# Kernel optimization log

Hardware: AMD Instinct MI355X
Metric: run time of the kernel (lower is better)

The kernel has to match this reference:

```python
import jax, jax.numpy as jnp
import numpy as np

B, T, DIM, H = 4, 2048, 1024, 16
NOPE, ROPE, VDIM, KVR = 128, 64, 128, 512
QKD = NOPE + ROPE  # 192
SCALE = QKD ** -0.5
THETA = 10000.0


def apply_rope(x, cos, sin):
    # x: (B, T, H, D) with interleaved (real, imag) pairs; cos/sin: (T, D//2)
    xr, xi = x[..., 0::2], x[..., 1::2]
    c = cos[None, :, None, :]
    s = sin[None, :, None, :]
    yr = xr * c - xi * s
    yi = xr * s + xi * c
    return jnp.stack([yr, yi], axis=-1).reshape(x.shape)


def rms_norm(x, eps=1e-6):
    return x * jax.lax.rsqrt(jnp.mean(x * x, axis=-1, keepdims=True) + eps)


def setup_inputs() -> dict:
    key = jax.random.key(0)
    ks = jax.random.split(key, 10)
    def lin(k, fan_in, fan_out):
        bound = 1.0 / np.sqrt(fan_in)
        kw, kb = jax.random.split(k)
        w = jax.random.uniform(kw, (fan_out, fan_in), jnp.float32, -bound, bound)
        b = jax.random.uniform(kb, (fan_out,), jnp.float32, -bound, bound)
        return w, b
    wq_w, wq_b = lin(ks[0], DIM, H * QKD)
    wkv_a_w, wkv_a_b = lin(ks[1], DIM, KVR + ROPE)
    wkv_b_w, wkv_b_b = lin(ks[2], KVR, H * (NOPE + VDIM))
    wo_w, wo_b = lin(ks[3], H * VDIM, DIM)
    x = jax.random.normal(ks[4], (B, T, DIM), jnp.float32)
    inv_freq = THETA ** (-jnp.arange(0, ROPE, 2, dtype=jnp.float32) / ROPE)  # (32,)
    ang = jnp.arange(T, dtype=jnp.float32)[:, None] * inv_freq[None, :]  # (T, 32)
    return {
        "x": x,
        "wq_w": wq_w, "wq_b": wq_b,
        "wkv_a_w": wkv_a_w, "wkv_a_b": wkv_a_b,
        "wkv_b_w": wkv_b_w, "wkv_b_b": wkv_b_b,
        "wo_w": wo_w, "wo_b": wo_b,
        "freqs_cos": jnp.cos(ang), "freqs_sin": jnp.sin(ang),
        "start_pos": 0,
    }


def reference(x, wq_w, wq_b, wkv_a_w, wkv_a_b, wkv_b_w, wkv_b_b, wo_w, wo_b,
              freqs_cos, freqs_sin, start_pos):
    b, t, _ = x.shape
    # Q projection, split into nope + rope parts
    q = (x @ wq_w.T + wq_b).reshape(b, t, H, QKD)
    q_nope, q_rope = q[..., :NOPE], q[..., NOPE:]
    q_rope = apply_rope(q_rope, freqs_cos, freqs_sin)
    q = jnp.concatenate([q_nope, q_rope], axis=-1)  # (B,T,H,192)
    # low-rank KV latent + shared rope key
    kv_a = x @ wkv_a_w.T + wkv_a_b  # (B,T,576)
    kv_lat, k_rope = kv_a[..., :KVR], kv_a[..., KVR:]
    k_rope = apply_rope(k_rope[:, :, None, :], freqs_cos, freqs_sin)  # (B,T,1,64)
    # decompress latent -> k_nope, v
    kv = (rms_norm(kv_lat) @ wkv_b_w.T + wkv_b_b).reshape(b, t, H, NOPE + VDIM)
    k_nope, v = kv[..., :NOPE], kv[..., NOPE:]
    k = jnp.concatenate([k_nope, jnp.broadcast_to(k_rope, (b, t, H, ROPE))], axis=-1)
    # causal SDPA (start_pos=0 prefill: cache[:end_pos] == current k/v)
    scores = jnp.einsum("bthd,bshd->bhts", q, k) * SCALE
    causal = jnp.tril(jnp.ones((t, t), dtype=bool))
    scores = jnp.where(causal[None, None], scores, jnp.finfo(scores.dtype).min)
    probs = jax.nn.softmax(scores, axis=-1)
    out = jnp.einsum("bhts,bshd->bthd", probs, v).reshape(b, t, H * VDIM)
    return out @ wo_w.T + wo_b
```

## Files before the change

### kernel.cpp

```cpp
#include <hip/hip_runtime.h>
#include <hip/hip_bf16.h>
#include <cmath>

#define B_    4
#define T_    2048
#define DIM_  1024
#define H_    16
#define NOPE_ 128
#define ROPE_ 64
#define VDIM_ 128
#define KVR_  512
#define QKD_  192
#define NTOK  (B_ * T_)

static constexpr float SCALE2_ = 0.07216878364870322f * 1.4426950408889634f;

typedef __attribute__((ext_vector_type(8))) unsigned short ushort8_t;
typedef __bf16 v8bf __attribute__((ext_vector_type(8)));
typedef float  v4f  __attribute__((ext_vector_type(4)));
typedef unsigned int v4u __attribute__((ext_vector_type(4)));

__device__ __forceinline__ float bf2f(unsigned short u) {
    return __uint_as_float(((unsigned int)u) << 16);
}
__device__ __forceinline__ unsigned short f2bf(float f) {
    unsigned int u = __float_as_uint(f);
    u += 0x7FFFu + ((u >> 16) & 1u);
    return (unsigned short)(u >> 16);
}
__device__ __forceinline__ unsigned short f2bf_hw(float f) {
    return __builtin_bit_cast(unsigned short, (__bf16)f);
}
__device__ __forceinline__ unsigned int cvt_pk_bf16(float lo, float hi) {
    unsigned int r;
    asm("v_cvt_pk_bf16_f32 %0, %1, %2" : "=v"(r) : "v"(lo), "v"(hi));
    return r;
}
__device__ __forceinline__ void store1(float* p, float v)          { *p = v; }
__device__ __forceinline__ void store1(__hip_bfloat16* p, float v) { *p = __float2bfloat16(v); }

__device__ __forceinline__ float exp2_hw(float x) {
    return __builtin_amdgcn_exp2f(x);
}

__device__ __forceinline__ void load_lds16(const void* g, void* l) {
    __builtin_amdgcn_global_load_lds(
        (const __attribute__((address_space(1))) void*)g,
        (__attribute__((address_space(3))) void*)l, 16, 0, 0);
}

__device__ __forceinline__ void cvt4(const float* s, __hip_bfloat16* d, int q4) {
    const int i = q4 * 4;
    const float4 v = *(const float4*)(s + i);
    ushort4 o;
    o.x = f2bf(v.x); o.y = f2bf(v.y); o.z = f2bf(v.z); o.w = f2bf(v.w);
    *(ushort4*)((unsigned short*)d + i) = o;
}

#define X4_   (NTOK*1024/4)
#define Q4_   (3072*1024/4)
#define KB4_  (4096*512/4)
#define O4_   (1024*2048/4)
#define A4_   (640*1024/4)
#define CVT_TOTAL (X4_ + Q4_ + KB4_ + O4_ + A4_)

__global__ __launch_bounds__(256) void cvt_all(
    const float* __restrict__ x,    const float* __restrict__ wq,
    const float* __restrict__ wkvb, const float* __restrict__ wo,
    const float* __restrict__ wkva, const float* __restrict__ wkva_bias,
    __hip_bfloat16* __restrict__ xb,    __hip_bfloat16* __restrict__ wqb,
    __hip_bfloat16* __restrict__ wkvbb, __hip_bfloat16* __restrict__ wob,
    __hip_bfloat16* __restrict__ wkvab, float* __restrict__ bias_pad)
{
    int idx = blockIdx.x * 256 + threadIdx.x;
    if (idx < X4_) { cvt4(x, xb, idx); return; }
    idx -= X4_;
    if (idx < Q4_) { cvt4(wq, wqb, idx); return; }
    idx -= Q4_;
    if (idx < KB4_) { cvt4(wkvb, wkvbb, idx); return; }
    idx -= KB4_;
    if (idx < O4_) { cvt4(wo, wob, idx); return; }
    idx -= O4_;
    if (idx < A4_) {
        const int i = idx * 4;
        ushort4 o;
        if (i < 576 * 1024) {
            const float4 v = *(const float4*)(wkva + i);
            o.x = f2bf(v.x); o.y = f2bf(v.y); o.z = f2bf(v.z); o.w = f2bf(v.w);
        } else {
            o.x = o.y = o.z = o.w = 0;
        }
        *(ushort4*)((unsigned short*)wkvab + i) = o;
        if (idx < 640) bias_pad[idx] = (idx < 576) ? wkva_bias[idx] : 0.0f;
    }
}

template <typename CT, int EPI>
__global__ __launch_bounds__(256) void gemm_mfma(
    const __hip_bfloat16* __restrict__ A, int lda,
    const __hip_bfloat16* __restrict__ W, int ldw,
    const float* __restrict__ bias,
    CT* __restrict__ C, int ldc, int K,
    unsigned short* __restrict__ kvf)
{
    __shared__ unsigned short smem[2 * 128 * 32];
    unsigned short* A_s = smem;
    unsigned short* B_s = smem + 128 * 32;

    const int tid  = threadIdx.x;
    const int ln   = tid & 63;
    const int wv   = tid >> 6;
    const int l15  = ln & 15;
    const int quad = ln >> 4;
    const int wm   = wv & 1, wn = wv >> 1;
    const int n0 = blockIdx.x * 128, m0 = blockIdx.y * 128;

    v4f acc[4][4] = {};

    for (int k0 = 0; k0 < K; k0 += 32) {
        __syncthreads();
        #pragma unroll
        for (int it = 0; it < 2; ++it) {
            const int idx = it * 256 + wv * 64;
            const int li  = idx + ln;
            const int row = li >> 2, ch = li & 3;
            load_lds16(A + (size_t)(m0 + row) * lda + k0 + ch * 8, &A_s[idx * 8]);
            load_lds16(W + (size_t)(n0 + row) * ldw + k0 + ch * 8, &B_s[idx * 8]);
        }
        __syncthreads();

        v8bf af[4], bf_[4];
        #pragma unroll
        for (int i = 0; i < 4; ++i) {
            af[i]  = *(const v8bf*)&A_s[(wm * 64 + i * 16 + l15) * 32 + quad * 8];
            bf_[i] = *(const v8bf*)&B_s[(wn * 64 + i * 16 + l15) * 32 + quad * 8];
        }
        #pragma unroll
        for (int i = 0; i < 4; ++i)
            #pragma unroll
            for (int j = 0; j < 4; ++j)
                acc[i][j] = __builtin_amdgcn_mfma_f32_16x16x32_bf16(
                                af[i], bf_[j], acc[i][j], 0, 0, 0);
    }

    if (EPI == 0) {
        #pragma unroll
        for (int i = 0; i < 4; ++i) {
            const int mrow = m0 + wm * 64 + i * 16 + quad * 4;
            #pragma unroll
            for (int j = 0; j < 4; ++j) {
                const int ncol = n0 + wn * 64 + j * 16 + l15;
                const float bb = bias[ncol];
                #pragma unroll
                for (int r = 0; r < 4; ++r)
                    store1(C + (size_t)(mrow + r) * ldc + ncol, acc[i][j][r] + bb);
            }
        }
    } else {
        const int head = n0 >> 8;
        const bool is_v = (n0 & 128) != 0;
        __syncthreads();
        #pragma unroll
        for (int p = 0; p < 2; ++p) {
            if (p) __syncthreads();
            if (wm == p) {
                #pragma unroll
                for (int i = 0; i < 4; ++i) {
                    #pragma unroll
                    for (int j = 0; j < 4; ++j) {
                        const int ncl = wn * 64 + j * 16 + l15;
                        const float bb = bias[n0 + ncl];
                        #pragma unroll
                        for (int r = 0; r < 4; ++r) {
                            const unsigned short v = f2bf(acc[i][j][r] + bb);
                            const int lnf = quad * 4 + r;
                            int off;
                            if (!is_v) {
                                const int s = ncl >> 5, qf = (ncl >> 3) & 3, e = ncl & 7;
                                off = (s * 4 + i) * 512 + (qf * 16 + lnf) * 8 + e;
                            } else {
                                const int nt = ncl >> 4, lnv = ncl & 15;
                                const int jj = i * 16 + lnf;
                                const int s2 = jj >> 5, qv = (jj >> 3) & 3, ev = jj & 7;
                                off = (nt * 2 + s2) * 512 + (qv * 16 + lnv) * 8 + ev;
                            }
                            smem[off] = v;
                        }
                    }
                }
            }
            __syncthreads();
            const size_t GT = (size_t)(m0 >> 6) + p;
            unsigned short* dst = kvf + ((GT * 16 + head) << 14) + (is_v ? 16 * 512 : 0);
            #pragma unroll
            for (int it = 0; it < 4; ++it) {
                const int u = (tid + it * 256) * 8;
                *(ushort8_t*)(dst + u) = *(const ushort8_t*)&smem[u];
            }
        }
    }
}

__global__ __launch_bounds__(256) void gemm_qkva(
    const __hip_bfloat16* __restrict__ A,
    const __hip_bfloat16* __restrict__ Wq, const float* __restrict__ biasq,
    __hip_bfloat16* __restrict__ Cq,
    const __hip_bfloat16* __restrict__ Wa, const float* __restrict__ biasa,
    __hip_bfloat16* __restrict__ Ca)
{
    __shared__ unsigned short smem[2 * 128 * 32];
    unsigned short* A_s = smem;
    unsigned short* B_s = smem + 128 * 32;

    const bool is_q = blockIdx.x < 24;
    const __hip_bfloat16* W = is_q ? Wq : Wa;
    const float* bias       = is_q ? biasq : biasa;
    __hip_bfloat16* C       = is_q ? Cq : Ca;
    const int ldc = is_q ? 3072 : 640;
    const int n0  = (is_q ? blockIdx.x : (blockIdx.x - 24)) * 128;
    const int m0  = blockIdx.y * 128;

    const int tid  = threadIdx.x;
    const int ln   = tid & 63;
    const int wv   = tid >> 6;
    const int l15  = ln & 15;
    const int quad = ln >> 4;
    const int wm   = wv & 1, wn = wv >> 1;

    v4f acc[4][4] = {};

    for (int k0 = 0; k0 < 1024; k0 += 32) {
        __syncthreads();
        #pragma unroll
        for (int it = 0; it < 2; ++it) {
            const int idx = it * 256 + wv * 64;
            const int li  = idx + ln;
            const int row = li >> 2, ch = li & 3;
            load_lds16(A + (size_t)(m0 + row) * 1024 + k0 + ch * 8, &A_s[idx * 8]);
            load_lds16(W + (size_t)(n0 + row) * 1024 + k0 + ch * 8, &B_s[idx * 8]);
        }
        __syncthreads();

        v8bf af[4], bf_[4];
        #pragma unroll
        for (int i = 0; i < 4; ++i) {
            af[i]  = *(const v8bf*)&A_s[(wm * 64 + i * 16 + l15) * 32 + quad * 8];
            bf_[i] = *(const v8bf*)&B_s[(wn * 64 + i * 16 + l15) * 32 + quad * 8];
        }
        #pragma unroll
        for (int i = 0; i < 4; ++i)
            #pragma unroll
            for (int j = 0; j < 4; ++j)
                acc[i][j] = __builtin_amdgcn_mfma_f32_16x16x32_bf16(
                                af[i], bf_[j], acc[i][j], 0, 0, 0);
    }

    #pragma unroll
    for (int i = 0; i < 4; ++i) {
        const int mrow = m0 + wm * 64 + i * 16 + quad * 4;
        #pragma unroll
        for (int j = 0; j < 4; ++j) {
            const int ncol = n0 + wn * 64 + j * 16 + l15;
            const float bb = bias[ncol];
            #pragma unroll
            for (int r = 0; r < 4; ++r)
                C[(size_t)(mrow + r) * ldc + ncol] = __float2bfloat16(acc[i][j][r] + bb);
        }
    }
}

__global__ __launch_bounds__(256) void rmsnorm_ropek(
    const __hip_bfloat16* __restrict__ kva,
    __hip_bfloat16* __restrict__ kvn,
    __hip_bfloat16* __restrict__ kr,
    const float* __restrict__ cs,
    const float* __restrict__ sn)
{
    const int tok = blockIdx.x;
    const int tid = threadIdx.x;
    const __hip_bfloat16* row = kva + (size_t)tok * 640;

    const float x0 = __bfloat162float(row[tid]);
    const float x1 = __bfloat162float(row[tid + 256]);
    float ss = x0*x0 + x1*x1;
    #pragma unroll
    for (int off = 32; off >= 1; off >>= 1)
        ss += __shfl_down(ss, off);

    __shared__ float red[4];
    __shared__ float scale_sh;
    if ((tid & 63) == 0) red[tid >> 6] = ss;
    __syncthreads();
    if (tid == 0) {
        const float tot = red[0] + red[1] + red[2] + red[3];
        scale_sh = rsqrtf(tot * (1.0f/512.0f) + 1e-6f);
    }
    __syncthreads();
    const float sc = scale_sh;
    kvn[(size_t)tok*512 + tid]       = __float2bfloat16(x0 * sc);
    kvn[(size_t)tok*512 + tid + 256] = __float2bfloat16(x1 * sc);

    if (tid < 32) {
        const int t = tok & (T_ - 1);
        const float c = cs[t*32 + tid];
        const float s = sn[t*32 + tid];
        const float xr = __bfloat162float(row[KVR_ + 2*tid]);
        const float xi = __bfloat162float(row[KVR_ + 2*tid + 1]);
        kr[(size_t)tok*64 + 2*tid]     = __float2bfloat16(xr * c - xi * s);
        kr[(size_t)tok*64 + 2*tid + 1] = __float2bfloat16(xr * s + xi * c);
    }
}

__device__ __forceinline__ void attn_stage_regs(
    v8bf* R,
    const unsigned short* __restrict__ kvf,
    const __hip_bfloat16* __restrict__ kr,
    size_t tokb, int j0, int h, int wv, int lane, int tid)
{
    const size_t GT = (tokb + j0) >> 6;
    const unsigned short* base = kvf + ((GT * 16 + h) << 14);
    #pragma unroll
    for (int i = 0; i < 4; ++i)
        R[i] = *(const v8bf*)(base + ((wv * 4 + i) << 9) + lane * 8);
    const int j = tid >> 3, dch = tid & 7;
    R[4] = *(const v8bf*)((const unsigned short*)kr + (tokb + j0 + j) * 64 + dch * 8);
}

__global__ __launch_bounds__(512, 2) void attn_mfma(
    const __hip_bfloat16* __restrict__ q,
    const unsigned short* __restrict__ kvf,
    const __hip_bfloat16* __restrict__ kr,
    const float* __restrict__ cs,
    const float* __restrict__ sn,
    __hip_bfloat16* __restrict__ att)
{
    __shared__ unsigned short KVf[40 * 512];

    const int tid  = threadIdx.x;
    const int lane = tid & 63;
    const int ln   = tid & 15;
    const int quad = (tid >> 4) & 3;
    const int wv   = tid >> 6;
    const int hf   = quad >> 1;
    const int p2   = quad & 1;

    const int bid  = (int)(blockIdx.x + 8u * blockIdx.y + 128u * blockIdx.z);
    const int half = bid >> 8;
    const int id2  = bid & 255;
    const int pr   = id2 & 3;
    const int h    = (id2 >> 2) & 15;
    const int b    = id2 >> 6;
    const int qt   = half ? pr : (7 - pr);

    const int q0 = qt * 256;
    const size_t tokb = (size_t)b * T_;

    v8bf qf[2][6];
    #pragma unroll
    for (int st = 0; st < 2; ++st) {
        const int trow = q0 + st*128 + wv*16 + ln;
        const __hip_bfloat16* qrow =
            q + (tokb + trow) * (size_t)(H_*QKD_) + h*QKD_;
        #pragma unroll
        for (int s = 0; s < 6; ++s) {
            ushort8_t raw = *(const ushort8_t*)(qrow + s*32 + quad*8);
            ushort8_t o;
            if (s < 4) {
                #pragma unroll
                for (int i = 0; i < 8; ++i)
                    o[i] = f2bf_hw(bf2f(raw[i]) * SCALE2_);
            } else {
                #pragma unroll
                for (int pp2 = 0; pp2 < 4; ++pp2) {
                    const int fi = (s-4)*16 + quad*4 + pp2;
                    const float c  = cs[trow*32 + fi];
                    const float sv = sn[trow*32 + fi];
                    const float xr = bf2f(raw[pp2*2]);
                    const float xi = bf2f(raw[pp2*2+1]);
                    o[pp2*2]   = f2bf_hw((xr*c - xi*sv) * SCALE2_);
                    o[pp2*2+1] = f2bf_hw((xr*sv + xi*c) * SCALE2_);
                }
            }
            qf[st][s] = __builtin_bit_cast(v8bf, o);
        }
    }

    v4f O[2][8];
    #pragma unroll
    for (int st = 0; st < 2; ++st)
        #pragma unroll
        for (int nt = 0; nt < 8; ++nt) O[st][nt] = (v4f){0.f, 0.f, 0.f, 0.f};
    float m_r[2] = {-1e30f, -1e30f};
    float l_r[2] = {0.0f, 0.0f};

    const int qmin0 = q0 + wv*16;
    const int qmin1 = q0 + 128 + wv*16;
    const int nkt = (q0 + 256) >> 6;

    const int slot0 = (wv < 4) ? (wv * 4) : (wv * 4 + 8);
    const int krj = tid >> 3, krd = tid & 7;
    const int krfrag = 16 + (krd >> 2) * 4 + (krj >> 4);
    const int kroff  = krfrag * 512 + ((krd & 3) * 16 + (krj & 15)) * 8;

    v8bf R[5];
    attn_stage_regs(R, kvf, kr, tokb, 0, h, wv, lane, tid);

    for (int kt = 0; kt < nkt; ++kt) {
        const int j0 = kt << 6;

        #pragma unroll
        for (int i = 0; i < 4; ++i)
            *(v8bf*)&KVf[(slot0 + i) * 512 + lane * 8] = R[i];
        *(v8bf*)&KVf[kroff] = R[4];
        __syncthreads();

        if (kt + 1 < nkt)
            attn_stage_regs(R, kvf, kr, tokb, j0 + 64, h, wv, lane, tid);

        const bool act0 = (j0 <= qmin0 + 15);
        const bool act1 = (j0 <= qmin1 + 15);

        if (act1) {
            v4f S[2][4];
            #pragma unroll
            for (int st = 0; st < 2; ++st)
                #pragma unroll
                for (int t = 0; t < 4; ++t) S[st][t] = (v4f){0.f, 0.f, 0.f, 0.f};
            __builtin_amdgcn_s_setprio(1);
            if (act0) {
                #pragma unroll
                for (int s = 0; s < 6; ++s)
                    #pragma unroll
                    for (int t = 0; t < 4; ++t) {
                        const v8bf kb = *(const v8bf*)&KVf[(s*4 + t)*512 + lane*8];
                        S[0][t] = __builtin_amdgcn_mfma_f32_16x16x32_bf16(kb, qf[0][s], S[0][t], 0, 0, 0);
                        S[1][t] = __builtin_amdgcn_mfma_f32_16x16x32_bf16(kb, qf[1][s], S[1][t], 0, 0, 0);
                    }
            } else {
                #pragma unroll
                for (int s = 0; s < 6; ++s)
                    #pragma unroll
                    for (int t = 0; t < 4; ++t) {
                        const v8bf kb = *(const v8bf*)&KVf[(s*4 + t)*512 + lane*8];
                        S[1][t] = __builtin_amdgcn_mfma_f32_16x16x32_bf16(kb, qf[1][s], S[1][t], 0, 0, 0);
                    }
            }
            __builtin_amdgcn_s_setprio(0);

            v8bf pfrag[2][2];
            #pragma unroll
            for (int st = 0; st < 2; ++st) {
                if (st == 0 && !act0) continue;
                const int qmin = (st == 0) ? qmin0 : qmin1;
                const int qrow = qmin + ln;
                if (j0 + 63 > qmin) {
                    #pragma unroll
                    for (int t = 0; t < 4; ++t) {
                        const int kbase = j0 + t*16 + quad*4;
                        #pragma unroll
                        for (int r = 0; r < 4; ++r)
                            if (kbase + r > qrow) S[st][t][r] = -1e30f;
                    }
                }
                float mx = S[st][0][0];
                #pragma unroll
                for (int t = 0; t < 4; ++t)
                    #pragma unroll
                    for (int r = 0; r < 4; ++r)
                        if (t || r) mx = fmaxf(mx, S[st][t][r]);
                mx = fmaxf(mx, __shfl_xor(mx, 16));
                mx = fmaxf(mx, __shfl_xor(mx, 32));
                const bool need = mx > m_r[st] + 8.0f;
                if (__any((int)need)) {
                    const float mn = fmaxf(m_r[st], mx);
                    const float alpha = exp2_hw(m_r[st] - mn);
                    m_r[st] = mn;
                    l_r[st] *= alpha;
                    #pragma unroll
                    for (int nt = 0; nt < 8; ++nt)
                        O[st][nt] *= alpha;
                }
                float rs = 0.0f;
                #pragma unroll
                for (int t = 0; t < 4; ++t)
                    #pragma unroll
                    for (int r = 0; r < 4; ++r) {
                        const float pp = exp2_hw(S[st][t][r] - m_r[st]);
                        S[st][t][r] = pp;
                        rs += pp;
                    }
                rs += __shfl_xor(rs, 16);
                rs += __shfl_xor(rs, 32);
                l_r[st] += rs;
                unsigned int pk[4][2];
                #pragma unroll
                for (int t = 0; t < 4; ++t)
                    #pragma unroll
                    for (int i = 0; i < 2; ++i)
                        pk[t][i] = cvt_pk_bf16(S[st][t][2*i], S[st][t][2*i+1]);
                #pragma unroll
                for (int s2 = 0; s2 < 2; ++s2) {
                    const unsigned int A0 = pk[2*s2][0],   A1 = pk[2*s2][1];
                    const unsigned int B0 = pk[2*s2+1][0], B1 = pk[2*s2+1][1];
                    const unsigned int sB0 = __shfl_xor(B0, 32), sB1 = __shfl_xor(B1, 32);
                    const unsigned int sA0 = __shfl_xor(A0, 32), sA1 = __shfl_xor(A1, 32);
                    const unsigned int U0 = hf ? sB0 : A0;
                    const unsigned int U1 = hf ? sB1 : A1;
                    const unsigned int V0 = hf ? B0 : sA0;
                    const unsigned int V1 = hf ? B1 : sA1;
                    const unsigned int xU0 = __shfl_xor(U0, 16), xU1 = __shfl_xor(U1, 16);
                    const unsigned int xV0 = __shfl_xor(V0, 16), xV1 = __shfl_xor(V1, 16);
                    v4u w;
                    w.x = p2 ? xV0 : U0;
                    w.y = p2 ? xV1 : U1;
                    w.z = p2 ? V0 : xU0;
                    w.w = p2 ? V1 : xU1;
                    pfrag[st][s2] = __builtin_bit_cast(v8bf, w);
                }
            }

            __builtin_amdgcn_s_setprio(1);
            #pragma unroll
            for (int s2 = 0; s2 < 2; ++s2) {
                if (act0) {
                    #pragma unroll
                    for (int nt = 0; nt < 8; ++nt) {
                        const v8bf vb = *(const v8bf*)&KVf[(24 + nt*2 + s2)*512 + lane*8];
                        O[0][nt] = __builtin_amdgcn_mfma_f32_16x16x32_bf16(vb, pfrag[0][s2], O[0][nt], 0, 0, 0);
                        O[1][nt] = __builtin_amdgcn_mfma_f32_16x16x32_bf16(vb, pfrag[1][s2], O[1][nt], 0, 0, 0);
                    }
                } else {
                    #pragma unroll
                    for (int nt = 0; nt < 8; ++nt) {
                        const v8bf vb = *(const v8bf*)&KVf[(24 + nt*2 + s2)*512 + lane*8];
                        O[1][nt] = __builtin_amdgcn_mfma_f32_16x16x32_bf16(vb, pfrag[1][s2], O[1][nt], 0, 0, 0);
                    }
                }
            }
            __builtin_amdgcn_s_setprio(0);
        }
        __syncthreads();
    }

    #pragma unroll
    for (int st = 0; st < 2; ++st) {
        const int qrow = q0 + st*128 + wv*16 + ln;
        const float inv = 1.0f / l_r[st];
        unsigned short* orow =
            (unsigned short*)att + (tokb + qrow) * (size_t)(H_*VDIM_) + h*VDIM_;
        #pragma unroll
        for (int nt = 0; nt < 8; ++nt) {
            #pragma unroll
            for (int rp = 0; rp < 2; ++rp) {
                const unsigned int w =
                    cvt_pk_bf16(O[st][nt][2*rp] * inv, O[st][nt][2*rp+1] * inv);
                *(unsigned int*)(orow + nt*16 + quad*4 + rp*2) = w;
            }
        }
    }
}

__global__ void fill_zero(float* p, int n) {
    int i = blockIdx.x * 256 + threadIdx.x;
    if (i < n) p[i] = 0.0f;
}

extern "C" void kernel_launch(void* const* d_in, const int* in_sizes, int n_in,
                              void* d_out, int out_size, void* d_ws, size_t ws_size,
                              hipStream_t stream)
{
    const float* x      = (const float*)d_in[0];
    const float* wq_w   = (const float*)d_in[1];
    const float* wq_b   = (const float*)d_in[2];
    const float* wkva_w = (const float*)d_in[3];
    const float* wkva_b = (const float*)d_in[4];
    const float* wkvb_w = (const float*)d_in[5];
    const float* wkvb_b = (const float*)d_in[6];
    const float* wo_w   = (const float*)d_in[7];
    const float* wo_b   = (const float*)d_in[8];
    const float* cs     = (const float*)d_in[9];
    const float* sn     = (const float*)d_in[10];

    const size_t q_b    = (size_t)NTOK * 3072 * 2;
    const size_t kvf_b  = (size_t)128 * 16 * 32 * 512 * 2;
    const size_t xb_b   = (size_t)NTOK * 1024 * 2;
    const size_t kvap_b = (size_t)NTOK * 640 * 2;
    const size_t kvn_b  = (size_t)NTOK * 512 * 2;
    const size_t wq_b_b = (size_t)3072 * 1024 * 2;
    const size_t wkva_b_b = (size_t)640 * 1024 * 2;
    const size_t wkvb_b_b = (size_t)4096 * 512 * 2;
    const size_t wo_b_b   = (size_t)1024 * 2048 * 2;
    const size_t bias_b   = 4096;
    const size_t need = q_b + kvf_b + xb_b + kvap_b + kvn_b +
                        wq_b_b + wkva_b_b + wkvb_b_b + wo_b_b + bias_b;

    if (ws_size < need) {
        fill_zero<<<(out_size + 255) / 256, 256, 0, stream>>>((float*)d_out, out_size);
        return;
    }

    char* p = (char*)d_ws;
    __hip_bfloat16* q    = (__hip_bfloat16*)p;             p += q_b;
    unsigned short* kvf  = (unsigned short*)p;             p += kvf_b;
    char*           dynr = p;
    __hip_bfloat16* xb   = (__hip_bfloat16*)p;             p += xb_b;
    __hip_bfloat16* kvap = (__hip_bfloat16*)p;             p += kvap_b;
    __hip_bfloat16* kvn  = (__hip_bfloat16*)p;             p += kvn_b;
    __hip_bfloat16* wq_bf = (__hip_bfloat16*)p;
    __hip_bfloat16* kr    = (__hip_bfloat16*)p;            p += wq_b_b;
    __hip_bfloat16* wkva_bf = (__hip_bfloat16*)p;          p += wkva_b_b;
    __hip_bfloat16* wkvb_bf = (__hip_bfloat16*)p;          p += wkvb_b_b;
    __hip_bfloat16* wo_bf   = (__hip_bfloat16*)p;          p += wo_b_b;
    float*          bias_pad = (float*)p;
    __hip_bfloat16* attb = (__hip_bfloat16*)dynr;
    float*          out  = (float*)d_out;

    cvt_all<<<CVT_TOTAL / 256, 256, 0, stream>>>(
        x, wq_w, wkvb_w, wo_w, wkva_w, wkva_b,
        xb, wq_bf, wkvb_bf, wo_bf, wkva_bf, bias_pad);

    gemm_qkva<<<dim3(29, NTOK/128), 256, 0, stream>>>(
        xb, wq_bf, wq_b, q, wkva_bf, bias_pad, kvap);

    rmsnorm_ropek<<<NTOK, 256, 0, stream>>>(kvap, kvn, kr, cs, sn);

    gemm_mfma<__hip_bfloat16, 1><<<dim3(4096/128, NTOK/128), 256, 0, stream>>>(
        kvn, 512, wkvb_bf, 512, wkvb_b, (( __hip_bfloat16*)nullptr), 0, 512, kvf);

    attn_mfma<<<dim3(T_/256, H_, B_), 512, 0, stream>>>(q, kvf, kr, cs, sn, attb);

    gemm_mfma<float, 0><<<dim3(1024/128, NTOK/128), 256, 0, stream>>>(
        attb, 2048, wo_bf, 2048, wo_b, out, 1024, 2048, nullptr);
}
```

Measured before the change: 479.2 us.

## Double-buffer attention KV tile in LDS and swizzle GEMM block order

The attention kernel now keeps two LDS buffers for the KV tile. The next tile is written into the alternate buffer after compute, which removes one __syncthreads per iteration and lets the write overlap with other waves' compute. Both GEMM kernels remap the flat block index with an XCD-style swizzle (stride 8) so that neighbouring tiles share L2 on the same die. Doubling LDS (80KB per block) may cut occupancy below 2 blocks/CU. The swizzle assumes the grid divides evenly by 8.

New measurement: 480.1 us. Within noise of the previous version (+0.2%).

```diff
diff --git a/kernel.cpp b/kernel.cpp
--- a/kernel.cpp
+++ b/kernel.cpp
@@ -113,7 +113,12 @@
     const int l15  = ln & 15;
     const int quad = ln >> 4;
     const int wm   = wv & 1, wn = wv >> 1;
-    const int n0 = blockIdx.x * 128, m0 = blockIdx.y * 128;
+
+    const int nwx = (int)gridDim.x, nwy = (int)gridDim.y;
+    const int flat = (int)blockIdx.x + nwx * (int)blockIdx.y;
+    const int cpx = (nwx * nwy) >> 3;
+    const int swz = (flat & 7) * cpx + (flat >> 3);
+    const int n0 = (swz / nwy) * 128, m0 = (swz % nwy) * 128;
 
     v4f acc[4][4] = {};
 
@@ -212,13 +217,17 @@
     unsigned short* A_s = smem;
     unsigned short* B_s = smem + 128 * 32;
 
-    const bool is_q = blockIdx.x < 24;
+    const int flat = (int)blockIdx.x + 29 * (int)blockIdx.y;
+    const int swz  = (flat & 7) * (1856 >> 3) + (flat >> 3);
+    const int xw   = swz / 64, yw = swz % 64;
+
+    const bool is_q = xw < 24;
     const __hip_bfloat16* W = is_q ? Wq : Wa;
     const float* bias       = is_q ? biasq : biasa;
     __hip_bfloat16* C       = is_q ? Cq : Ca;
     const int ldc = is_q ? 3072 : 640;
-    const int n0  = (is_q ? blockIdx.x : (blockIdx.x - 24)) * 128;
-    const int m0  = blockIdx.y * 128;
+    const int n0  = (is_q ? xw : (xw - 24)) * 128;
+    const int m0  = yw * 128;
 
     const int tid  = threadIdx.x;
     const int ln   = tid & 63;
@@ -334,7 +343,7 @@
     const float* __restrict__ sn,
     __hip_bfloat16* __restrict__ att)
 {
-    __shared__ unsigned short KVf[40 * 512];
+    __shared__ unsigned short KVf[2][40 * 512];
 
     const int tid  = threadIdx.x;
     const int lane = tid & 63;
@@ -404,14 +413,19 @@
 
     v8bf R[5];
     attn_stage_regs(R, kvf, kr, tokb, 0, h, wv, lane, tid);
+    {
+        unsigned short* Kw = KVf[0];
+        #pragma unroll
+        for (int i = 0; i < 4; ++i)
+            *(v8bf*)&Kw[(slot0 + i) * 512 + lane * 8] = R[i];
+        *(v8bf*)&Kw[kroff] = R[4];
+    }
 
     for (int kt = 0; kt < nkt; ++kt) {
         const int j0 = kt << 6;
-
-        #pragma unroll
-        for (int i = 0; i < 4; ++i)
-            *(v8bf*)&KVf[(slot0 + i) * 512 + lane * 8] = R[i];
-        *(v8bf*)&KVf[kroff] = R[4];
+        const int cur = kt & 1;
+        const unsigned short* Kb = KVf[cur];
+
         __syncthreads();
 
         if (kt + 1 < nkt)
@@ -432,7 +446,7 @@
                 for (int s = 0; s < 6; ++s)
                     #pragma unroll
                     for (int t = 0; t < 4; ++t) {
-                        const v8bf kb = *(const v8bf*)&KVf[(s*4 + t)*512 + lane*8];
+                        const v8bf kb = *(const v8bf*)&Kb[(s*4 + t)*512 + lane*8];
                         S[0][t] = __builtin_amdgcn_mfma_f32_16x16x32_bf16(kb, qf[0][s], S[0][t], 0, 0, 0);
                         S[1][t] = __builtin_amdgcn_mfma_f32_16x16x32_bf16(kb, qf[1][s], S[1][t], 0, 0, 0);
                     }
@@ -441,7 +455,7 @@
                 for (int s = 0; s < 6; ++s)
                     #pragma unroll
                     for (int t = 0; t < 4; ++t) {
-                        const v8bf kb = *(const v8bf*)&KVf[(s*4 + t)*512 + lane*8];
+                        const v8bf kb = *(const v8bf*)&Kb[(s*4 + t)*512 + lane*8];
                         S[1][t] = __builtin_amdgcn_mfma_f32_16x16x32_bf16(kb, qf[1][s], S[1][t], 0, 0, 0);
                     }
             }
@@ -525,21 +539,28 @@
                 if (act0) {
                     #pragma unroll
                     for (int nt = 0; nt < 8; ++nt) {
-                        const v8bf vb = *(const v8bf*)&KVf[(24 + nt*2 + s2)*512 + lane*8];
+                        const v8bf vb = *(const v8bf*)&Kb[(24 + nt*2 + s2)*512 + lane*8];
                         O[0][nt] = __builtin_amdgcn_mfma_f32_16x16x32_bf16(vb, pfrag[0][s2], O[0][nt], 0, 0, 0);
                         O[1][nt] = __builtin_amdgcn_mfma_f32_16x16x32_bf16(vb, pfrag[1][s2], O[1][nt], 0, 0, 0);
                     }
                 } else {
                     #pragma unroll
                     for (int nt = 0; nt < 8; ++nt) {
-                        const v8bf vb = *(const v8bf*)&KVf[(24 + nt*2 + s2)*512 + lane*8];
+                        const v8bf vb = *(const v8bf*)&Kb[(24 + nt*2 + s2)*512 + lane*8];
                         O[1][nt] = __builtin_amdgcn_mfma_f32_16x16x32_bf16(vb, pfrag[1][s2], O[1][nt], 0, 0, 0);
                     }
                 }
             }
             __builtin_amdgcn_s_setprio(0);
         }
-        __syncthreads();
+
+        if (kt + 1 < nkt) {
+            unsigned short* Kw = KVf[cur ^ 1];
+            #pragma unroll
+            for (int i = 0; i < 4; ++i)
+                *(v8bf*)&Kw[(slot0 + i) * 512 + lane * 8] = R[i];
+            *(v8bf*)&Kw[kroff] = R[4];
+        }
     }
 
     #pragma unroll
```
